# Performance work log

Hardware: AMD Instinct MI355X
Metric: run time of the kernel (lower is better)

The kernel has to match this reference:

```python
import jax, jax.numpy as jnp
import numpy as np

N = 100000
E = 1600000
IN_C = 128
HEADS = 4
HEAD_D = 32  # out_channels(128) // heads(4)


def setup_inputs() -> dict:
    key = jax.random.key(0)
    k1, k2, k3, k4, k5, k6 = jax.random.split(key, 6)
    x = jax.random.normal(k1, (N, IN_C), dtype=jnp.float32)
    edge_index = jax.random.randint(k2, (2, E), 0, N, dtype=jnp.int64)
    edge_weight = jax.random.uniform(k3, (E,), dtype=jnp.float32)
    # params: linear weight stored as [in, H*D] so forward is x @ W (torch does x @ weight.T)
    W = jax.random.normal(k4, (IN_C, HEADS * HEAD_D), dtype=jnp.float32) * (1.0 / np.sqrt(IN_C))
    att_src = jax.random.normal(k5, (HEADS, HEAD_D), dtype=jnp.float32) * 0.1
    att_dst = jax.random.normal(k6, (HEADS, HEAD_D), dtype=jnp.float32) * 0.1
    return {"x": x, "W": W, "att_src": att_src, "att_dst": att_dst,
            "edge_weight": edge_weight, "edge_index": edge_index, "num_nodes": N}


def reference(x, W, att_src, att_dst, edge_weight, edge_index, num_nodes):
    H, D = att_src.shape
    xw = (x @ W).reshape(-1, H, D)                       # [N, H, D]
    row, col = edge_index[0], edge_index[1]
    a_src = jnp.einsum('nhd,hd->nh', xw, att_src)        # [N, H]
    a_dst = jnp.einsum('nhd,hd->nh', xw, att_dst)        # [N, H]
    alpha = jax.nn.leaky_relu(a_src[row] + a_dst[col], negative_slope=0.2)  # [E, H]
    # segment softmax over edges grouped by row (destination of aggregation)
    amax = jax.ops.segment_max(alpha, row, num_segments=num_nodes)          # [N, H]
    amax = jnp.where(jnp.isfinite(amax), amax, 0.0)      # empty segments -> 0 (matches torch init)
    alpha = jnp.exp(alpha - amax[row])
    asum = jax.ops.segment_sum(alpha, row, num_segments=num_nodes)          # [N, H]
    alpha = alpha / (asum[row] + 1e-16)
    msg = xw[col] * alpha[..., None]                     # [E, H, D]
    out = jax.ops.segment_sum(msg, row, num_segments=num_nodes)             # [N, H, D]
    return out.reshape(num_nodes, H * D)
```

## Files before the change

kernel.cpp:

```cpp
#include <hip/hip_runtime.h>
#include <math.h>


typedef _Float16 half4 __attribute__((ext_vector_type(4)));
typedef _Float16 half8 __attribute__((ext_vector_type(8)));
typedef float    f32x4 __attribute__((ext_vector_type(4)));

#define PCHUNK   4096
#define NB_SHIFT 8
#define BCAP     4864

__device__ __forceinline__ float lrelu_exp(float v) {
    return __expf(fmaxf(v, 0.2f * v));
}

__global__ __launch_bounds__(128) void k_prep(const float* __restrict__ W,
                                              const float* __restrict__ att_src,
                                              const float* __restrict__ att_dst,
                                              _Float16* __restrict__ Wa) {
    int n = blockIdx.x;
    int k = threadIdx.x;
    float v;
    if (n < 128) {
        v = W[(size_t)k * 128 + n];
    } else if (n < 136) {
        int h = (n - 128) & 3;
        const float* att = (n < 132) ? att_src : att_dst;
        float s = 0.f;
        #pragma unroll
        for (int d = 0; d < 32; ++d)
            s += W[(size_t)k * 128 + h * 32 + d] * att[h * 32 + d];
        v = s;
    } else {
        v = 0.f;
    }
    Wa[n * 128 + k] = (_Float16)v;
}

__device__ __forceinline__ _Float16* lds_ptr(_Float16* base, int r, int kf16) {
    int g = (kf16 >> 3) ^ (r & 7);
    return base + r * 128 + g * 8 + (kf16 & 7);
}

__global__ __launch_bounds__(256) void k_fat(const float* __restrict__ x,
                                             const _Float16* __restrict__ Wa,
                                             _Float16* __restrict__ xwh,
                                             float* __restrict__ a_src,
                                             float* __restrict__ a_dst, int N,
                                             const int* __restrict__ eidx,
                                             int* __restrict__ bctr,
                                             unsigned* __restrict__ rec, int E,
                                             int nPart, int stride) {
    __shared__ __align__(16) char smem[57360];
    int bid = blockIdx.x;
    int t = threadIdx.x;
    int lane = t & 63, wv = t >> 6;
    int q = bid / stride, r = bid - q * stride;

    if (r == 0 && q < nPart) {
        unsigned long long* buf = (unsigned long long*)smem;
        unsigned* sbuf = (unsigned*)(smem + 32768);
        int* hist = (int*)(smem + 49152);
        int* excl = hist + 512;
        int* gbase = excl + 512;
        int* cur = gbase + 512;
        int* wtot = cur + 512;
        int e0 = q * PCHUNK;
        int nE = E - e0; if (nE > PCHUNK) nE = PCHUNK;
        hist[t] = 0; hist[t + 256] = 0;
        __syncthreads();
        for (int i = t; i < nE; i += 256) {
            int row = __builtin_nontemporal_load(&eidx[e0 + i]);
            int col = __builtin_nontemporal_load(&eidx[E + e0 + i]);
            buf[i] = ((unsigned long long)(unsigned)col << 32) | (unsigned)row;
            atomicAdd(&hist[row >> NB_SHIFT], 1);
        }
        __syncthreads();
        int h0 = hist[2 * t], h1 = hist[2 * t + 1];
        int s = h0 + h1, sc = s;
        #pragma unroll
        for (int off = 1; off < 64; off <<= 1) {
            int v = __shfl_up(sc, off);
            if (lane >= off) sc += v;
        }
        if (lane == 63) wtot[wv] = sc;
        __syncthreads();
        if (t == 0) {
            int run = 0;
            #pragma unroll
            for (int i = 0; i < 4; ++i) { int tmp = wtot[i]; wtot[i] = run; run += tmp; }
        }
        __syncthreads();
        int incl = sc + wtot[wv];
        excl[2 * t]     = incl - s;
        excl[2 * t + 1] = incl - h1;
        cur[2 * t]      = incl - s;
        cur[2 * t + 1]  = incl - h1;
        gbase[2 * t]     = h0 ? atomicAdd(&bctr[2 * t], h0) : 0;
        gbase[2 * t + 1] = h1 ? atomicAdd(&bctr[2 * t + 1], h1) : 0;
        __syncthreads();
        unsigned long long myrec[PCHUNK / 256];
        #pragma unroll
        for (int k = 0; k < PCHUNK / 256; ++k) {
            int i = t + k * 256;
            if (i < nE) myrec[k] = buf[i];
        }
        __syncthreads();
        unsigned short* bkt16 = (unsigned short*)buf;
        #pragma unroll
        for (int k = 0; k < PCHUNK / 256; ++k) {
            int i = t + k * 256;
            if (i < nE) {
                unsigned long long rr = myrec[k];
                int row = (int)(unsigned)rr;
                int b = row >> NB_SHIFT;
                int dst = atomicAdd(&cur[b], 1);
                sbuf[dst] = ((unsigned)(rr >> 32) << 8) | ((unsigned)row & 255u);
                bkt16[dst] = (unsigned short)b;
            }
        }
        __syncthreads();
        for (int j = t; j < nE; j += 256) {
            unsigned rr = sbuf[j];
            int b = bkt16[j];
            int off = gbase[b] + (j - excl[b]);
            if (off < BCAP)
                __builtin_nontemporal_store(rr, &rec[(size_t)b * BCAP + off]);
        }
        return;
    }

    int nb = q + (r ? 1 : 0); if (nb > nPart) nb = nPart;
    int gid = bid - nb;
    _Float16* Xs = (_Float16*)smem;
    _Float16* Ws = (_Float16*)(smem + 16384);
    int lm = lane & 15, lg = lane >> 4;
    int row0 = gid * 64;

    #pragma unroll
    for (int i = 0; i < 9; ++i) {
        int f = (i * 256 + t) * 8;
        int nr = f >> 7, kc = f & 127;
        *(half8*)lds_ptr(Ws, nr, kc) = *(const half8*)&Wa[f];
    }
    #pragma unroll
    for (int i = 0; i < 4; ++i) {
        int f = (i * 256 + t) * 8;
        int rr = f >> 7, kc = f & 127;
        int gr = row0 + rr; if (gr >= N) gr = N - 1;
        float4 v0 = *(const float4*)&x[(size_t)gr * 128 + kc];
        float4 v1 = *(const float4*)&x[(size_t)gr * 128 + kc + 4];
        half8 hv;
        hv[0] = (_Float16)v0.x; hv[1] = (_Float16)v0.y;
        hv[2] = (_Float16)v0.z; hv[3] = (_Float16)v0.w;
        hv[4] = (_Float16)v1.x; hv[5] = (_Float16)v1.y;
        hv[6] = (_Float16)v1.z; hv[7] = (_Float16)v1.w;
        *(half8*)lds_ptr(Xs, rr, kc) = hv;
    }
    __syncthreads();

    f32x4 acc[9];
    #pragma unroll
    for (int nn = 0; nn < 9; ++nn) acc[nn] = (f32x4){0.f, 0.f, 0.f, 0.f};

    #pragma unroll
    for (int kk = 0; kk < 4; ++kk) {
        int kb = kk * 32 + lg * 8;
        half8 a0 = *(const half8*)lds_ptr(Xs, wv * 16 + lm, kb);
        #pragma unroll
        for (int nn = 0; nn < 9; ++nn) {
            half8 b = *(const half8*)lds_ptr(Ws, nn * 16 + lm, kb);
            acc[nn] = __builtin_amdgcn_mfma_f32_16x16x32_f16(a0, b, acc[nn], 0, 0, 0);
        }
    }

    #pragma unroll
    for (int reg = 0; reg < 4; ++reg) {
        int row = row0 + wv * 16 + lg * 4 + reg;
        if (row < N) {
            #pragma unroll
            for (int nn = 0; nn < 8; ++nn)
                xwh[(size_t)row * 128 + nn * 16 + lm] = (_Float16)acc[nn][reg];
            float lv = acc[8][reg];
            if (lm < 4)      a_src[(size_t)row * 4 + lm]       = lv;
            else if (lm < 8) a_dst[(size_t)row * 4 + (lm - 4)] = lv;
        }
    }
}

__global__ __launch_bounds__(1024) void k_csr(const unsigned* __restrict__ rec,
                                              const int* __restrict__ bctr,
                                              int2* __restrict__ rseg,
                                              int* __restrict__ csr_col, int N) {
    __shared__ int cnt[256], cur[256];
    __shared__ int wtot[4];
    int b = blockIdx.x;
    int rs = b << NB_SHIFT;
    int t = threadIdx.x;
    int lane = t & 63, wv = t >> 6;
    if (t < 256) cnt[t] = 0;
    __syncthreads();
    int m = bctr[b]; if (m > BCAP) m = BCAP;
    const unsigned* rr = &rec[(size_t)b * BCAP];
    for (int i = t; i < m; i += 1024) {
        unsigned r = rr[i];
        atomicAdd(&cnt[r & 255u], 1);
    }
    __syncthreads();
    int c = (t < 256) ? cnt[t] : 0;
    int sc = c;
    #pragma unroll
    for (int off = 1; off < 64; off <<= 1) {
        int v = __shfl_up(sc, off);
        if (lane >= off) sc += v;
    }
    if (t < 256 && lane == 63) wtot[wv] = sc;
    __syncthreads();
    if (t == 0) {
        int run = 0;
        #pragma unroll
        for (int i = 0; i < 4; ++i) { int tmp = wtot[i]; wtot[i] = run; run += tmp; }
    }
    __syncthreads();
    if (t < 256) {
        int ex = sc + wtot[wv] - c;
        cur[t] = ex;
        int n = rs + t;
        if (n < N) {
            int2 sg;
            sg.x = b * BCAP + ex;
            sg.y = b * BCAP + ex + c;
            rseg[n] = sg;
        }
    }
    __syncthreads();
    for (int i = t; i < m; i += 1024) {
        unsigned r = rr[i];
        int slot = atomicAdd(&cur[r & 255u], 1);
        csr_col[b * BCAP + slot] = (int)(r >> 8);
    }
}

__global__ __launch_bounds__(256) void k_agg(const int2* __restrict__ rseg,
                                             const int* __restrict__ csr_col,
                                             const float* __restrict__ a_src,
                                             const float* __restrict__ a_dst,
                                             const _Float16* __restrict__ xwh,
                                             float* __restrict__ out,
                                             int n0, int n1) {
    int lane = threadIdx.x & 63;
    int n = n0 + blockIdx.x * 4 + (threadIdx.x >> 6);
    if (n >= n1) return;
    int2 seg = rseg[n];
    int beg = seg.x, end = seg.y;
    int q = lane >> 4;
    int l = lane & 15;
    int h = l >> 2;
    float s_n = a_src[(size_t)n * 4 + h];
    float acc[8] = {0, 0, 0, 0, 0, 0, 0, 0};
    float ws = 0.f;

    for (int w0 = beg; w0 < end; w0 += 64) {
        int rem = end - w0; if (rem > 64) rem = 64;
        int cc = (lane < rem) ? __builtin_nontemporal_load(&csr_col[w0 + lane]) : 0;
        int j = 0;
        for (; j + 16 <= rem; j += 16) {
            int c[4]; float ad[4]; half8 xv[4];
            #pragma unroll
            for (int u = 0; u < 4; ++u) c[u] = __shfl(cc, j + u * 4 + q);
            #pragma unroll
            for (int u = 0; u < 4; ++u) {
                ad[u] = a_dst[(size_t)c[u] * 4 + h];
                xv[u] = *(const half8*)&xwh[(size_t)c[u] * 128 + (l << 3)];
            }
            #pragma unroll
            for (int u = 0; u < 4; ++u) {
                float w = lrelu_exp(s_n + ad[u]);
                ws += w;
                #pragma unroll
                for (int k = 0; k < 8; ++k)
                    acc[k] += w * (float)xv[u][k];
            }
        }
        if (j < rem) {
            int c[4]; float m[4]; float ad[4]; half8 xv[4];
            #pragma unroll
            for (int u = 0; u < 4; ++u) {
                int r = j + u * 4 + q;
                c[u] = __shfl(cc, r);
                m[u] = (r < rem) ? 1.f : 0.f;
            }
            #pragma unroll
            for (int u = 0; u < 4; ++u) {
                ad[u] = a_dst[(size_t)c[u] * 4 + h];
                xv[u] = *(const half8*)&xwh[(size_t)c[u] * 128 + (l << 3)];
            }
            #pragma unroll
            for (int u = 0; u < 4; ++u) {
                float w = m[u] * lrelu_exp(s_n + ad[u]);
                ws += w;
                #pragma unroll
                for (int k = 0; k < 8; ++k)
                    acc[k] += w * (float)xv[u][k];
            }
        }
    }

    #pragma unroll
    for (int k = 0; k < 8; ++k) {
        acc[k] += __shfl_xor(acc[k], 16);
        acc[k] += __shfl_xor(acc[k], 32);
    }
    ws += __shfl_xor(ws, 16);
    ws += __shfl_xor(ws, 32);
    if (q == 0) {
        float inv = 1.0f / (ws + 1e-16f);
        f32x4 o0 = {acc[0] * inv, acc[1] * inv, acc[2] * inv, acc[3] * inv};
        f32x4 o1 = {acc[4] * inv, acc[5] * inv, acc[6] * inv, acc[7] * inv};
        __builtin_nontemporal_store(o0, (f32x4*)&out[(size_t)n * 128 + (l << 3)]);
        __builtin_nontemporal_store(o1, (f32x4*)&out[(size_t)n * 128 + (l << 3) + 4]);
    }
}

extern "C" void kernel_launch(void* const* d_in, const int* in_sizes, int n_in,
                              void* d_out, int out_size, void* d_ws, size_t ws_size,
                              hipStream_t stream) {
    const float* x       = (const float*)d_in[0];
    const float* W       = (const float*)d_in[1];
    const float* att_src = (const float*)d_in[2];
    const float* att_dst = (const float*)d_in[3];
    const int* eidx      = (const int*)d_in[5];
    int N = in_sizes[0] / 128;
    int E = in_sizes[4];
    float* out = (float*)d_out;

    char* p = (char*)d_ws;
    auto alloc = [&](size_t bytes) {
        char* r = p;
        p += (bytes + 255) & ~(size_t)255;
        return r;
    };
    int nbuckets = (N + 255) >> NB_SHIFT;
    _Float16* xwh  = (_Float16*)alloc((size_t)N * 128 * 2);
    float* a_src   = (float*)alloc((size_t)N * 4 * 4);
    float* a_dst   = (float*)alloc((size_t)N * 4 * 4);
    int*   bctr    = (int*)  alloc(512 * 4);
    unsigned* rec  = (unsigned*)alloc((size_t)nbuckets * BCAP * 4);
    int2*  rseg    = (int2*) alloc((size_t)N * 8);
    int*   csr_col = (int*)  alloc((size_t)nbuckets * BCAP * 4);
    _Float16* Wa   = (_Float16*)alloc(144 * 128 * 2);

    int nPart = (E + PCHUNK - 1) / PCHUNK;
    int nGemm = (N + 63) / 64;
    int total = nPart + nGemm;
    int stride = total / nPart; if (stride < 1) stride = 1;

    (void)hipMemsetAsync(bctr, 0, 512 * 4, stream);
    k_prep<<<144, 128, 0, stream>>>(W, att_src, att_dst, Wa);
    k_fat<<<total, 256, 0, stream>>>(x, Wa, xwh, a_src, a_dst, N,
                                     eidx, bctr, rec, E, nPart, stride);
    k_csr<<<nbuckets, 1024, 0, stream>>>(rec, bctr, rseg, csr_col, N);
    int half = N / 2;
    k_agg<<<(half + 3) / 4, 256, 0, stream>>>(rseg, csr_col, a_src, a_dst, xwh, out, 0, half);
    k_agg<<<(N - half + 3) / 4, 256, 0, stream>>>(rseg, csr_col, a_src, a_dst, xwh, out, half, N);
}
```

Measured before the change: 251.4 us.

## Loop GEMM blocks over multiple row tiles, shrink CSR blocks, split aggregation in three

The fused partition/GEMM kernel now places all partition blocks first and gives each GEMM block 8 consecutive 64-row tiles. The W tile is loaded into LDS once per block, and the next tile's x rows are prefetched into registers while the current tile runs through MFMA. The CSR build kernel drops from 1024 to 256 threads per block, so no threads sit idle in the scan, and the aggregation launch is split into three kernels instead of two. The changes target repeated W staging and launch or occupancy overheads. In exchange there are far fewer GEMM blocks, which may leave CUs idle and lose the interleaving of partition and GEMM blocks that the old stride scheme provided.

New measurement: 251.4 us. About the same (+0.0%).

```diff
diff --git a/kernel.cpp b/kernel.cpp
--- a/kernel.cpp
+++ b/kernel.cpp
@@ -9,6 +9,7 @@
 #define PCHUNK   4096
 #define NB_SHIFT 8
 #define BCAP     4864
+#define GTILES   8
 
 __device__ __forceinline__ float lrelu_exp(float v) {
     return __expf(fmaxf(v, 0.2f * v));
@@ -50,14 +51,13 @@
                                              const int* __restrict__ eidx,
                                              int* __restrict__ bctr,
                                              unsigned* __restrict__ rec, int E,
-                                             int nPart, int stride) {
+                                             int nPart) {
     __shared__ __align__(16) char smem[57360];
     int bid = blockIdx.x;
     int t = threadIdx.x;
     int lane = t & 63, wv = t >> 6;
-    int q = bid / stride, r = bid - q * stride;
-
-    if (r == 0 && q < nPart) {
+
+    if (bid < nPart) {
         unsigned long long* buf = (unsigned long long*)smem;
         unsigned* sbuf = (unsigned*)(smem + 32768);
         int* hist = (int*)(smem + 49152);
@@ -65,7 +65,7 @@
         int* gbase = excl + 512;
         int* cur = gbase + 512;
         int* wtot = cur + 512;
-        int e0 = q * PCHUNK;
+        int e0 = bid * PCHUNK;
         int nE = E - e0; if (nE > PCHUNK) nE = PCHUNK;
         hist[t] = 0; hist[t + 256] = 0;
         __syncthreads();
@@ -130,12 +130,13 @@
         return;
     }
 
-    int nb = q + (r ? 1 : 0); if (nb > nPart) nb = nPart;
-    int gid = bid - nb;
+    int gid = bid - nPart;
     _Float16* Xs = (_Float16*)smem;
     _Float16* Ws = (_Float16*)(smem + 16384);
     int lm = lane & 15, lg = lane >> 4;
-    int row0 = gid * 64;
+    int brow0 = gid * (64 * GTILES);
+    int ntiles = (N - brow0 + 63) >> 6;
+    if (ntiles > GTILES) ntiles = GTILES;
 
     #pragma unroll
     for (int i = 0; i < 9; ++i) {
@@ -143,78 +144,97 @@
         int nr = f >> 7, kc = f & 127;
         *(half8*)lds_ptr(Ws, nr, kc) = *(const half8*)&Wa[f];
     }
+
+    int srow[4], skc[4];
     #pragma unroll
     for (int i = 0; i < 4; ++i) {
         int f = (i * 256 + t) * 8;
-        int rr = f >> 7, kc = f & 127;
-        int gr = row0 + rr; if (gr >= N) gr = N - 1;
-        float4 v0 = *(const float4*)&x[(size_t)gr * 128 + kc];
-        float4 v1 = *(const float4*)&x[(size_t)gr * 128 + kc + 4];
-        half8 hv;
-        hv[0] = (_Float16)v0.x; hv[1] = (_Float16)v0.y;
-        hv[2] = (_Float16)v0.z; hv[3] = (_Float16)v0.w;
-        hv[4] = (_Float16)v1.x; hv[5] = (_Float16)v1.y;
-        hv[6] = (_Float16)v1.z; hv[7] = (_Float16)v1.w;
-        *(half8*)lds_ptr(Xs, rr, kc) = hv;
-    }
-    __syncthreads();
-
-    f32x4 acc[9];
-    #pragma unroll
-    for (int nn = 0; nn < 9; ++nn) acc[nn] = (f32x4){0.f, 0.f, 0.f, 0.f};
-
-    #pragma unroll
-    for (int kk = 0; kk < 4; ++kk) {
-        int kb = kk * 32 + lg * 8;
-        half8 a0 = *(const half8*)lds_ptr(Xs, wv * 16 + lm, kb);
-        #pragma unroll
-        for (int nn = 0; nn < 9; ++nn) {
-            half8 b = *(const half8*)lds_ptr(Ws, nn * 16 + lm, kb);
-            acc[nn] = __builtin_amdgcn_mfma_f32_16x16x32_f16(a0, b, acc[nn], 0, 0, 0);
-        }
-    }
-
-    #pragma unroll
-    for (int reg = 0; reg < 4; ++reg) {
-        int row = row0 + wv * 16 + lg * 4 + reg;
-        if (row < N) {
-            #pragma unroll
-            for (int nn = 0; nn < 8; ++nn)
-                xwh[(size_t)row * 128 + nn * 16 + lm] = (_Float16)acc[nn][reg];
-            float lv = acc[8][reg];
-            if (lm < 4)      a_src[(size_t)row * 4 + lm]       = lv;
-            else if (lm < 8) a_dst[(size_t)row * 4 + (lm - 4)] = lv;
-        }
-    }
-}
-
-__global__ __launch_bounds__(1024) void k_csr(const unsigned* __restrict__ rec,
-                                              const int* __restrict__ bctr,
-                                              int2* __restrict__ rseg,
-                                              int* __restrict__ csr_col, int N) {
+        srow[i] = f >> 7;
+        skc[i]  = f & 127;
+    }
+    float4 xr0[4], xr1[4];
+    #pragma unroll
+    for (int i = 0; i < 4; ++i) {
+        int gr = brow0 + srow[i]; if (gr >= N) gr = N - 1;
+        xr0[i] = *(const float4*)&x[(size_t)gr * 128 + skc[i]];
+        xr1[i] = *(const float4*)&x[(size_t)gr * 128 + skc[i] + 4];
+    }
+
+    for (int g = 0; g < ntiles; ++g) {
+        int row0 = brow0 + g * 64;
+        __syncthreads();
+        #pragma unroll
+        for (int i = 0; i < 4; ++i) {
+            half8 hv;
+            hv[0] = (_Float16)xr0[i].x; hv[1] = (_Float16)xr0[i].y;
+            hv[2] = (_Float16)xr0[i].z; hv[3] = (_Float16)xr0[i].w;
+            hv[4] = (_Float16)xr1[i].x; hv[5] = (_Float16)xr1[i].y;
+            hv[6] = (_Float16)xr1[i].z; hv[7] = (_Float16)xr1[i].w;
+            *(half8*)lds_ptr(Xs, srow[i], skc[i]) = hv;
+        }
+        __syncthreads();
+        if (g + 1 < ntiles) {
+            #pragma unroll
+            for (int i = 0; i < 4; ++i) {
+                int gr = row0 + 64 + srow[i]; if (gr >= N) gr = N - 1;
+                xr0[i] = *(const float4*)&x[(size_t)gr * 128 + skc[i]];
+                xr1[i] = *(const float4*)&x[(size_t)gr * 128 + skc[i] + 4];
+            }
+        }
+        f32x4 acc[9];
+        #pragma unroll
+        for (int nn = 0; nn < 9; ++nn) acc[nn] = (f32x4){0.f, 0.f, 0.f, 0.f};
+        #pragma unroll
+        for (int kk = 0; kk < 4; ++kk) {
+            int kb = kk * 32 + lg * 8;
+            half8 a0 = *(const half8*)lds_ptr(Xs, wv * 16 + lm, kb);
+            #pragma unroll
+            for (int nn = 0; nn < 9; ++nn) {
+                half8 b = *(const half8*)lds_ptr(Ws, nn * 16 + lm, kb);
+                acc[nn] = __builtin_amdgcn_mfma_f32_16x16x32_f16(a0, b, acc[nn], 0, 0, 0);
+            }
+        }
+        #pragma unroll
+        for (int reg = 0; reg < 4; ++reg) {
+            int row = row0 + wv * 16 + lg * 4 + reg;
+            if (row < N) {
+                #pragma unroll
+                for (int nn = 0; nn < 8; ++nn)
+                    xwh[(size_t)row * 128 + nn * 16 + lm] = (_Float16)acc[nn][reg];
+                float lv = acc[8][reg];
+                if (lm < 4)      a_src[(size_t)row * 4 + lm]       = lv;
+                else if (lm < 8) a_dst[(size_t)row * 4 + (lm - 4)] = lv;
+            }
+        }
+    }
+}
+
+__global__ __launch_bounds__(256) void k_csr(const unsigned* __restrict__ rec,
+                                             const int* __restrict__ bctr,
+                                             int2* __restrict__ rseg,
+                                             int* __restrict__ csr_col, int N) {
     __shared__ int cnt[256], cur[256];
     __shared__ int wtot[4];
     int b = blockIdx.x;
     int rs = b << NB_SHIFT;
     int t = threadIdx.x;
     int lane = t & 63, wv = t >> 6;
-    if (t < 256) cnt[t] = 0;
+    cnt[t] = 0;
     __syncthreads();
     int m = bctr[b]; if (m > BCAP) m = BCAP;
     const unsigned* rr = &rec[(size_t)b * BCAP];
-    for (int i = t; i < m; i += 1024) {
+    for (int i = t; i < m; i += 256) {
         unsigned r = rr[i];
         atomicAdd(&cnt[r & 255u], 1);
     }
     __syncthreads();
-    int c = (t < 256) ? cnt[t] : 0;
-    int sc = c;
+    int c = cnt[t], sc = c;
     #pragma unroll
     for (int off = 1; off < 64; off <<= 1) {
         int v = __shfl_up(sc, off);
         if (lane >= off) sc += v;
     }
-    if (t < 256 && lane == 63) wtot[wv] = sc;
+    if (lane == 63) wtot[wv] = sc;
     __syncthreads();
     if (t == 0) {
         int run = 0;
@@ -222,19 +242,17 @@
         for (int i = 0; i < 4; ++i) { int tmp = wtot[i]; wtot[i] = run; run += tmp; }
     }
     __syncthreads();
-    if (t < 256) {
-        int ex = sc + wtot[wv] - c;
-        cur[t] = ex;
-        int n = rs + t;
-        if (n < N) {
-            int2 sg;
-            sg.x = b * BCAP + ex;
-            sg.y = b * BCAP + ex + c;
-            rseg[n] = sg;
-        }
-    }
-    __syncthreads();
-    for (int i = t; i < m; i += 1024) {
+    int ex = sc + wtot[wv] - c;
+    cur[t] = ex;
+    int n = rs + t;
+    if (n < N) {
+        int2 sg;
+        sg.x = b * BCAP + ex;
+        sg.y = b * BCAP + ex + c;
+        rseg[n] = sg;
+    }
+    __syncthreads();
+    for (int i = t; i < m; i += 256) {
         unsigned r = rr[i];
         int slot = atomicAdd(&cur[r & 255u], 1);
         csr_col[b * BCAP + slot] = (int)(r >> 8);
@@ -350,17 +368,16 @@
     int*   csr_col = (int*)  alloc((size_t)nbuckets * BCAP * 4);
     _Float16* Wa   = (_Float16*)alloc(144 * 128 * 2);
 
-    int nPart = (E + PCHUNK - 1) / PCHUNK;
-    int nGemm = (N + 63) / 64;
-    int total = nPart + nGemm;
-    int stride = total / nPart; if (stride < 1) stride = 1;
+    int nPart  = (E + PCHUNK - 1) / PCHUNK;
+    int nGemmB = (N + 64 * GTILES - 1) / (64 * GTILES);
 
     (void)hipMemsetAsync(bctr, 0, 512 * 4, stream);
     k_prep<<<144, 128, 0, stream>>>(W, att_src, att_dst, Wa);
-    k_fat<<<total, 256, 0, stream>>>(x, Wa, xwh, a_src, a_dst, N,
-                                     eidx, bctr, rec, E, nPart, stride);
-    k_csr<<<nbuckets, 1024, 0, stream>>>(rec, bctr, rseg, csr_col, N);
-    int half = N / 2;
-    k_agg<<<(half + 3) / 4, 256, 0, stream>>>(rseg, csr_col, a_src, a_dst, xwh, out, 0, half);
-    k_agg<<<(N - half + 3) / 4, 256, 0, stream>>>(rseg, csr_col, a_src, a_dst, xwh, out, half, N);
-}
+    k_fat<<<nPart + nGemmB, 256, 0, stream>>>(x, Wa, xwh, a_src, a_dst, N,
+                                              eidx, bctr, rec, E, nPart);
+    k_csr<<<nbuckets, 256, 0, stream>>>(rec, bctr, rseg, csr_col, N);
+    int third = N / 3;
+    k_agg<<<(third + 3) / 4, 256, 0, stream>>>(rseg, csr_col, a_src, a_dst, xwh, out, 0, third);
+    k_agg<<<(third + 3) / 4, 256, 0, stream>>>(rseg, csr_col, a_src, a_dst, xwh, out, third, 2 * third);
+    k_agg<<<(N - 2 * third + 3) / 4, 256, 0, stream>>>(rseg, csr_col, a_src, a_dst, xwh, out, 2 * third, N);
+}
```
